# Optimization experiments

Hardware: AMD Instinct MI355X
Metric: run time of the kernel (lower is better)

Reference implementation:

```python
import jax, jax.numpy as jnp
import numpy as np

N_USER, N_SPOT, D = 100000, 50000, 128
E_VISIT, E_REV, E_NEAR = 500000, 500000, 200000
P_DROP = 0.1


def _glorot(k, fan_in, fan_out):
    lim = jnp.sqrt(6.0 / (fan_in + fan_out))
    return jax.random.uniform(k, (fan_in, fan_out), jnp.float32, -lim, lim)


def setup_inputs() -> dict:
    key = jax.random.key(0)
    ks = jax.random.split(key, 14)
    return {
        "x_user": jax.random.normal(ks[0], (N_USER, D), jnp.float32),
        "x_spot": jax.random.normal(ks[1], (N_SPOT, D), jnp.float32),
        "W_visit_src": _glorot(ks[2], D, D),   # user side of (user,visit,spot)
        "W_visit_tgt": _glorot(ks[3], D, D),   # spot side of (user,visit,spot)
        "W_rev_src": _glorot(ks[4], D, D),     # spot side of (spot,visited_by,user)
        "W_rev_tgt": _glorot(ks[5], D, D),     # user side of (spot,visited_by,user)
        "W_near_src": _glorot(ks[6], D, D),    # (spot,near,spot)
        "W_near_tgt": _glorot(ks[7], D, D),
        "visit_src": jax.random.randint(ks[8], (E_VISIT,), 0, N_USER, jnp.int64),
        "visit_dst": jax.random.randint(ks[9], (E_VISIT,), 0, N_SPOT, jnp.int64),
        "rev_src": jax.random.randint(ks[10], (E_REV,), 0, N_SPOT, jnp.int64),
        "rev_dst": jax.random.randint(ks[11], (E_REV,), 0, N_USER, jnp.int64),
        "near_src": jax.random.randint(ks[12], (E_NEAR,), 0, N_SPOT, jnp.int64),
        "near_dst": jax.random.randint(ks[13], (E_NEAR,), 0, N_SPOT, jnp.int64),
    }


def _scatter_mean(vals, idx, n_seg):
    # scatter(..., reduce='mean') into zeros: empty segments stay 0
    s = jax.ops.segment_sum(vals, idx, num_segments=n_seg)
    c = jax.ops.segment_sum(jnp.ones((vals.shape[0],), vals.dtype), idx, num_segments=n_seg)
    return s / jnp.maximum(c, 1.0)[:, None]


def _edge_type(x_src, x_tgt, W_src, W_tgt, src_idx, dst_idx, n_tgt, dkey):
    src_p = x_src @ W_src                      # [N_src, D]
    tgt_p = x_tgt @ W_tgt                      # [N_tgt, D]
    g = src_p[src_idx]                         # gather per edge [E, D]
    keep = jax.random.bernoulli(dkey, 1.0 - P_DROP, g.shape)
    g = jnp.where(keep, g / (1.0 - P_DROP), jnp.zeros_like(g))  # dropout (training)
    return tgt_p + _scatter_mean(g, dst_idx, n_tgt)


def reference(x_user, x_spot, W_visit_src, W_visit_tgt, W_rev_src, W_rev_tgt,
              W_near_src, W_near_tgt, visit_src, visit_dst, rev_src, rev_dst,
              near_src, near_dst):
    dk = jax.random.key(1)
    spot_a = _edge_type(x_user, x_spot, W_visit_src, W_visit_tgt,
                        visit_src, visit_dst, N_SPOT, jax.random.fold_in(dk, 0))
    user_a = _edge_type(x_spot, x_user, W_rev_src, W_rev_tgt,
                        rev_src, rev_dst, N_USER, jax.random.fold_in(dk, 1))
    spot_b = _edge_type(x_spot, x_spot, W_near_src, W_near_tgt,
                        near_src, near_dst, N_SPOT, jax.random.fold_in(dk, 2))
    # div: spot receives from 2 edge types, user from 1
    out_user = jax.nn.relu(user_a / 1.0)
    out_spot = jax.nn.relu((spot_a + spot_b) / 2.0)
    # ReLU=True applies a second relu (no-op after the first, kept for faithfulness)
    return jax.nn.relu(out_user), jax.nn.relu(out_spot)
```

## Files before the change

### kernel.cpp

```cpp
#include <hip/hip_runtime.h>
#include <stdint.h>

#define DF 128
typedef unsigned short ushort_t;
typedef __attribute__((ext_vector_type(8))) short short8v;
typedef __attribute__((ext_vector_type(4))) float f32x4;

__host__ __device__ __forceinline__ unsigned rotl32(unsigned v, int r) {
  return __builtin_rotateleft32(v, (unsigned)r);
}

__host__ __device__ __forceinline__ void threefry2x32(
    unsigned k0, unsigned k1, unsigned c0, unsigned c1,
    unsigned& o0, unsigned& o1) {
  unsigned kx = k0 ^ k1 ^ 0x1BD11BDAu;
  unsigned x0 = c0 + k0;
  unsigned x1 = c1 + k1;
#define TF_R(r) { x0 += x1; x1 = rotl32(x1, r); x1 ^= x0; }
  TF_R(13) TF_R(15) TF_R(26) TF_R(6)
  x0 += k1; x1 += kx + 1u;
  TF_R(17) TF_R(29) TF_R(16) TF_R(24)
  x0 += kx; x1 += k0 + 2u;
  TF_R(13) TF_R(15) TF_R(26) TF_R(6)
  x0 += k0; x1 += k1 + 3u;
  TF_R(17) TF_R(29) TF_R(16) TF_R(24)
  x0 += k1; x1 += kx + 4u;
  TF_R(13) TF_R(15) TF_R(26) TF_R(6)
  x0 += kx; x1 += k0 + 5u;
#undef TF_R
  o0 = x0; o1 = x1;
}

#define KEEP_THR 0xE6666600u

__device__ __forceinline__ ushort_t f2bf(float f) {
  unsigned u = __float_as_uint(f);
  unsigned r = (u + 0x7fffu + ((u >> 16) & 1u)) >> 16;
  return (ushort_t)r;
}
__device__ __forceinline__ float bf2f(unsigned h) {
  return __uint_as_float(h << 16);
}
__device__ __forceinline__ unsigned umin_u(unsigned a, unsigned b) {
  return a < b ? a : b;
}

#define WT(k, c) sm_u[(k) * 136 + (c)]
#define CTB(r, c) sm_u[(r) * 144 + (c)]
#define CTF(r, c) sm_f[(r) * 68 + (c)]

__device__ __forceinline__ void gemm_core(
    const float* __restrict__ X, const float* __restrict__ W1,
    const float* __restrict__ W2, bool sumW, int M, int rbase,
    ushort_t* sm_u, f32x4 acc[2][8]) {
  const int t = threadIdx.x;
  const int lane = t & 63;
  const int w = t >> 6;
  const int lr = lane & 15;
  const int kg = lane >> 4;

#pragma unroll
  for (int i = 0; i < 16; ++i) {
    int q = t + i * 256;
    int k = q >> 5;
    int c4 = (q & 31) * 4;
    float4 wv = *reinterpret_cast<const float4*>(&W1[k * DF + c4]);
    if (sumW) {
      float4 w2 = *reinterpret_cast<const float4*>(&W2[k * DF + c4]);
      wv.x += w2.x; wv.y += w2.y; wv.z += w2.z; wv.w += w2.w;
    }
    WT(c4 + 0, k) = f2bf(wv.x);
    WT(c4 + 1, k) = f2bf(wv.y);
    WT(c4 + 2, k) = f2bf(wv.z);
    WT(c4 + 3, k) = f2bf(wv.w);
  }
  __syncthreads();

#pragma unroll
  for (int rg = 0; rg < 2; ++rg)
#pragma unroll
    for (int n = 0; n < 8; ++n) acc[rg][n] = (f32x4){0.f, 0.f, 0.f, 0.f};

#pragma unroll
  for (int kt = 0; kt < 4; ++kt) {
    const int kb = kt * 32 + kg * 8;
    short8v a[2];
#pragma unroll
    for (int rg = 0; rg < 2; ++rg) {
      int r = rbase + w * 32 + rg * 16 + lr;
      float4 x0 = make_float4(0.f, 0.f, 0.f, 0.f);
      float4 x1 = x0;
      if (r < M) {
        x0 = *reinterpret_cast<const float4*>(&X[(size_t)r * DF + kb]);
        x1 = *reinterpret_cast<const float4*>(&X[(size_t)r * DF + kb + 4]);
      }
      short8v av;
      av[0] = (short)f2bf(x0.x); av[1] = (short)f2bf(x0.y);
      av[2] = (short)f2bf(x0.z); av[3] = (short)f2bf(x0.w);
      av[4] = (short)f2bf(x1.x); av[5] = (short)f2bf(x1.y);
      av[6] = (short)f2bf(x1.z); av[7] = (short)f2bf(x1.w);
      a[rg] = av;
    }
#pragma unroll
    for (int n = 0; n < 8; ++n) {
      short8v b = *reinterpret_cast<const short8v*>(&WT(n * 16 + lr, kb));
#pragma unroll
      for (int rg = 0; rg < 2; ++rg)
        acc[rg][n] = __builtin_amdgcn_mfma_f32_16x16x32_bf16(a[rg], b, acc[rg][n], 0, 0, 0);
    }
  }
}

__global__ __launch_bounds__(256) void proj3_gemm(
    const float* __restrict__ x_user, const float* __restrict__ x_spot,
    const float* __restrict__ Wv, const float* __restrict__ Wr,
    const float* __restrict__ Wn, int n_user, int n_spot,
    ushort_t* __restrict__ pv, ushort_t* __restrict__ pr,
    ushort_t* __restrict__ pn, int gbU, int gbS) {
  __shared__ __align__(16) ushort_t sm_u[18432];
  const int b = blockIdx.x;
  const float* X; const float* W; ushort_t* out; int M; int rbase;
  if (b < gbU)            { X = x_user; W = Wv; out = pv; M = n_user; rbase = b * 128; }
  else if (b < gbU + gbS) { X = x_spot; W = Wr; out = pr; M = n_spot; rbase = (b - gbU) * 128; }
  else                    { X = x_spot; W = Wn; out = pn; M = n_spot; rbase = (b - gbU - gbS) * 128; }

  f32x4 acc[2][8];
  gemm_core(X, W, nullptr, false, M, rbase, sm_u, acc);

  const int t = threadIdx.x;
  const int lane = t & 63;
  const int w = t >> 6;
  const int lr = lane & 15;
  const int kg = lane >> 4;

  __syncthreads();
#pragma unroll
  for (int rg = 0; rg < 2; ++rg) {
    const int rowb = w * 32 + rg * 16 + kg * 4;
#pragma unroll
    for (int n = 0; n < 8; ++n) {
      const int col = n * 16 + lr;
#pragma unroll
      for (int j = 0; j < 4; ++j) CTB(rowb + j, col) = f2bf(acc[rg][n][j]);
    }
  }
  __syncthreads();
#pragma unroll
  for (int i = 0; i < 8; ++i) {
    const int u = t + i * 256;
    const int row = u >> 4, ch = u & 15;
    const int grow = rbase + row;
    if (grow < M)
      *reinterpret_cast<uint4*>(&out[(size_t)grow * DF + ch * 8]) =
          *reinterpret_cast<const uint4*>(&CTB(row, ch * 8));
  }
}

__global__ __launch_bounds__(256) void final2_gemm(
    const float* __restrict__ x_user, const float* __restrict__ x_spot,
    const float* __restrict__ Wrt, const float* __restrict__ Wvt,
    const float* __restrict__ Wnt, int n_user, int n_spot,
    float* __restrict__ out_user, float* __restrict__ out_spot,
    const ushort_t* __restrict__ mean_u, const ushort_t* __restrict__ mean_sv,
    const ushort_t* __restrict__ mean_sn, int gbU) {
  __shared__ __align__(16) ushort_t sm_u[17408];
  float* sm_f_raw = reinterpret_cast<float*>(sm_u);
#define sm_f sm_f_raw
  const int b = blockIdx.x;
  const bool epi2 = (b >= gbU);
  const float* X; const float* W1; const float* W2; float* outF;
  const ushort_t* m1; const ushort_t* m2; int M; int rbase;
  if (!epi2) {
    X = x_user; W1 = Wrt; W2 = nullptr; outF = out_user;
    m1 = mean_u; m2 = nullptr; M = n_user; rbase = b * 128;
  } else {
    X = x_spot; W1 = Wvt; W2 = Wnt; outF = out_spot;
    m1 = mean_sv; m2 = mean_sn; M = n_spot; rbase = (b - gbU) * 128;
  }

  f32x4 acc[2][8];
  gemm_core(X, W1, W2, epi2, M, rbase, sm_u, acc);

  const int t = threadIdx.x;
  const int lane = t & 63;
  const int w = t >> 6;
  const int lr = lane & 15;
  const int kg = lane >> 4;

#pragma unroll
  for (int h = 0; h < 2; ++h) {
    __syncthreads();
#pragma unroll
    for (int rg = 0; rg < 2; ++rg) {
      const int rowb = w * 32 + rg * 16 + kg * 4;
#pragma unroll
      for (int n2 = 0; n2 < 4; ++n2) {
        const int n = h * 4 + n2;
        const int col = n2 * 16 + lr;
#pragma unroll
        for (int j = 0; j < 4; ++j) CTF(rowb + j, col) = acc[rg][n][j];
      }
    }
    __syncthreads();
#pragma unroll
    for (int i = 0; i < 8; ++i) {
      const int u = t + i * 256;
      const int row = u >> 4;
      const int c4 = (u & 15) * 4;
      const int grow = rbase + row;
      if (grow < M) {
        const float4 vv = *reinterpret_cast<const float4*>(&CTF(row, c4));
        const int col = h * 64 + c4;
        const uint2 mb = *reinterpret_cast<const uint2*>(&m1[(size_t)grow * DF + col]);
        float a0 = bf2f(mb.x & 0xffffu), a1 = bf2f(mb.x >> 16);
        float a2 = bf2f(mb.y & 0xffffu), a3 = bf2f(mb.y >> 16);
        float4 r;
        if (!epi2) {
          r.x = fmaxf(vv.x + a0, 0.f);
          r.y = fmaxf(vv.y + a1, 0.f);
          r.z = fmaxf(vv.z + a2, 0.f);
          r.w = fmaxf(vv.w + a3, 0.f);
        } else {
          const uint2 nb = *reinterpret_cast<const uint2*>(&m2[(size_t)grow * DF + col]);
          r.x = fmaxf(0.5f * (vv.x + a0 + bf2f(nb.x & 0xffffu)), 0.f);
          r.y = fmaxf(0.5f * (vv.y + a1 + bf2f(nb.x >> 16)), 0.f);
          r.z = fmaxf(0.5f * (vv.z + a2 + bf2f(nb.y & 0xffffu)), 0.f);
          r.w = fmaxf(0.5f * (vv.w + a3 + bf2f(nb.y >> 16)), 0.f);
        }
        *reinterpret_cast<float4*>(&outF[(size_t)grow * DF + col]) = r;
      }
    }
  }
#undef sm_f
}

__global__ __launch_bounds__(256) void hist3(
    const int* __restrict__ vd, const int* __restrict__ rd,
    const int* __restrict__ nd, unsigned* __restrict__ deg_all,
    int Ev, int Er, int En, int segU, int segN) {
  int i = blockIdx.x * 256 + threadIdx.x;
  if (i < Ev) atomicAdd(&deg_all[vd[i]], 1u);
  else if (i < Ev + Er) atomicAdd(&deg_all[segU + rd[i - Ev]], 1u);
  else if (i < Ev + Er + En) atomicAdd(&deg_all[segN + nd[i - Ev - Er]], 1u);
}

#define SCAN_E 2048

__global__ __launch_bounds__(256) void scanA(
    const unsigned* __restrict__ deg, unsigned* __restrict__ bsum, int NT) {
  __shared__ unsigned sm[256];
  const int t = threadIdx.x;
  const int base = blockIdx.x * SCAN_E + t * 8;
  unsigned s = 0;
#pragma unroll
  for (int j = 0; j < 8; ++j) {
    int i = base + j;
    s += (i < NT) ? deg[i] : 0u;
  }
  sm[t] = s;
  __syncthreads();
  for (int off = 128; off; off >>= 1) {
    if (t < off) sm[t] += sm[t + off];
    __syncthreads();
  }
  if (t == 0) bsum[blockIdx.x] = sm[0];
}

__global__ __launch_bounds__(1024) void scanB(
    unsigned* __restrict__ bsum, unsigned* __restrict__ rp_all,
    int nb, int NT) {
  __shared__ unsigned sm[1024];
  const int t = threadIdx.x;
  unsigned v = (t < nb) ? bsum[t] : 0u;
  sm[t] = v;
  __syncthreads();
  for (int off = 1; off < 1024; off <<= 1) {
    unsigned u = (t >= off) ? sm[t - off] : 0u;
    __syncthreads();
    sm[t] += u;
    __syncthreads();
  }
  if (t < nb) bsum[t] = sm[t] - v;
  if (t == nb - 1) rp_all[NT] = sm[t];
}

__global__ __launch_bounds__(256) void scanC(
    const unsigned* __restrict__ deg, const unsigned* __restrict__ bsum,
    unsigned* __restrict__ rp, unsigned* __restrict__ cur, int NT) {
  __shared__ unsigned sm[256];
  const int t = threadIdx.x;
  const int base = blockIdx.x * SCAN_E + t * 8;
  unsigned vals[8];
  unsigned s = 0;
#pragma unroll
  for (int j = 0; j < 8; ++j) {
    int i = base + j;
    vals[j] = (i < NT) ? deg[i] : 0u;
    s += vals[j];
  }
  sm[t] = s;
  __syncthreads();
  for (int off = 1; off < 256; off <<= 1) {
    unsigned u = (t >= off) ? sm[t - off] : 0u;
    __syncthreads();
    sm[t] += u;
    __syncthreads();
  }
  unsigned run = bsum[blockIdx.x] + sm[t] - s;
#pragma unroll
  for (int j = 0; j < 8; ++j) {
    int i = base + j;
    if (i < NT) { rp[i] = run; cur[i] = run; }
    run += vals[j];
  }
}

__global__ __launch_bounds__(256) void fill3(
    const int* __restrict__ vs, const int* __restrict__ vd,
    const int* __restrict__ rs, const int* __restrict__ rd,
    const int* __restrict__ ns, const int* __restrict__ nd,
    unsigned* __restrict__ cur_all, uint2* __restrict__ es_all,
    int Ev, int Er, int En, int segU, int segN) {
  int i = blockIdx.x * 256 + threadIdx.x;
  if (i < Ev) {
    unsigned slot = atomicAdd(&cur_all[vd[i]], 1u);
    es_all[slot] = make_uint2((unsigned)i, (unsigned)vs[i]);
  } else if (i < Ev + Er) {
    int e = i - Ev;
    unsigned slot = atomicAdd(&cur_all[segU + rd[e]], 1u);
    es_all[slot] = make_uint2((unsigned)e, (unsigned)rs[e]);
  } else if (i < Ev + Er + En) {
    int e = i - Ev - Er;
    unsigned slot = atomicAdd(&cur_all[segN + nd[e]], 1u);
    es_all[slot] = make_uint2((unsigned)e, (unsigned)ns[e]);
  }
}

__global__ __launch_bounds__(256) void gather_reduce_all(
    const ushort_t* __restrict__ proj_v, const ushort_t* __restrict__ proj_r,
    const ushort_t* __restrict__ proj_n, const uint2* __restrict__ es,
    const unsigned* __restrict__ rp, ushort_t* __restrict__ accum_all,
    int NT, int segU, int segN, unsigned emax,
    unsigned kv0, unsigned kv1, unsigned kr0, unsigned kr1,
    unsigned kn0, unsigned kn1) {
  const int lane = threadIdx.x & 63;
  int d = blockIdx.x * 4 + (threadIdx.x >> 6);
  d = __builtin_amdgcn_readfirstlane(d);
  if (d >= NT) return;

  const ushort_t* proj;
  unsigned k0, k1;
  if (d < segU)      { proj = proj_v; k0 = kv0; k1 = kv1; }
  else if (d < segN) { proj = proj_r; k0 = kr0; k1 = kr1; }
  else               { proj = proj_n; k0 = kn0; k1 = kn1; }

  const unsigned b0 = __builtin_amdgcn_readfirstlane(rp[d]);
  const unsigned n  = __builtin_amdgcn_readfirstlane(rp[d + 1]) - b0;

  const bool hi = lane >= 32;
  const unsigned l31 = (unsigned)(lane & 31);
  const unsigned voff8 = l31 * 8u;

  const unsigned npairs = n >> 1;
  const unsigned odd = n & 1u;

  uint2 P0 = es[umin_u(b0, emax)];
  uint2 P1 = es[umin_u(b0 + 1u, emax)];
  unsigned eA = __builtin_amdgcn_readfirstlane(P0.x);
  unsigned sA = __builtin_amdgcn_readfirstlane(P0.y);
  unsigned eB = __builtin_amdgcn_readfirstlane(P1.x);
  unsigned sB = __builtin_amdgcn_readfirstlane(P1.y);

  float a0 = 0.f, a1 = 0.f, a2 = 0.f, a3 = 0.f;

  for (unsigned p = 0; p < npairs; ++p) {
    const unsigned src = hi ? sB : sA;
    const unsigned eid = hi ? eB : eA;
    const uint2 g = *reinterpret_cast<const uint2*>(
        reinterpret_cast<const char*>(proj) + ((size_t)src << 8) + voff8);
    uint2 Pn0 = es[umin_u(b0 + 2u * p + 2u, emax)];
    uint2 Pn1 = es[umin_u(b0 + 2u * p + 3u, emax)];

    const unsigned cb = eid * 128u + l31 * 4u;
    unsigned r0a, r0b, r1a, r1b, r2a, r2b, r3a, r3b;
    threefry2x32(k0, k1, 0u, cb + 0u, r0a, r0b);
    threefry2x32(k0, k1, 0u, cb + 1u, r1a, r1b);
    threefry2x32(k0, k1, 0u, cb + 2u, r2a, r2b);
    threefry2x32(k0, k1, 0u, cb + 3u, r3a, r3b);
    const float m0 = ((r0a ^ r0b) < KEEP_THR) ? (1.0f / 0.9f) : 0.f;
    const float m1 = ((r1a ^ r1b) < KEEP_THR) ? (1.0f / 0.9f) : 0.f;
    const float m2 = ((r2a ^ r2b) < KEEP_THR) ? (1.0f / 0.9f) : 0.f;
    const float m3 = ((r3a ^ r3b) < KEEP_THR) ? (1.0f / 0.9f) : 0.f;
    a0 = fmaf(__uint_as_float(g.x << 16), m0, a0);
    a1 = fmaf(__uint_as_float(g.x & 0xffff0000u), m1, a1);
    a2 = fmaf(__uint_as_float(g.y << 16), m2, a2);
    a3 = fmaf(__uint_as_float(g.y & 0xffff0000u), m3, a3);

    eA = __builtin_amdgcn_readfirstlane(Pn0.x);
    sA = __builtin_amdgcn_readfirstlane(Pn0.y);
    eB = __builtin_amdgcn_readfirstlane(Pn1.x);
    sB = __builtin_amdgcn_readfirstlane(Pn1.y);
  }

  if (odd) {
    const uint2 g = *reinterpret_cast<const uint2*>(
        reinterpret_cast<const char*>(proj) + ((size_t)sA << 8) + voff8);
    const unsigned cb = eA * 128u + l31 * 4u;
    unsigned r0a, r0b, r1a, r1b, r2a, r2b, r3a, r3b;
    threefry2x32(k0, k1, 0u, cb + 0u, r0a, r0b);
    threefry2x32(k0, k1, 0u, cb + 1u, r1a, r1b);
    threefry2x32(k0, k1, 0u, cb + 2u, r2a, r2b);
    threefry2x32(k0, k1, 0u, cb + 3u, r3a, r3b);
    const float sc = hi ? 0.f : (1.0f / 0.9f);
    const float m0 = ((r0a ^ r0b) < KEEP_THR) ? sc : 0.f;
    const float m1 = ((r1a ^ r1b) < KEEP_THR) ? sc : 0.f;
    const float m2 = ((r2a ^ r2b) < KEEP_THR) ? sc : 0.f;
    const float m3 = ((r3a ^ r3b) < KEEP_THR) ? sc : 0.f;
    a0 = fmaf(__uint_as_float(g.x << 16), m0, a0);
    a1 = fmaf(__uint_as_float(g.x & 0xffff0000u), m1, a1);
    a2 = fmaf(__uint_as_float(g.y << 16), m2, a2);
    a3 = fmaf(__uint_as_float(g.y & 0xffff0000u), m3, a3);
  }

  a0 += __shfl_xor(a0, 32);
  a1 += __shfl_xor(a1, 32);
  a2 += __shfl_xor(a2, 32);
  a3 += __shfl_xor(a3, 32);

  const float inv = 1.0f / fmaxf((float)n, 1.0f);
  const float u0 = hi ? a2 : a0;
  const float u1 = hi ? a3 : a1;
  const unsigned pk =
      ((unsigned)f2bf(u0 * inv)) | (((unsigned)f2bf(u1 * inv)) << 16);
  unsigned* out = reinterpret_cast<unsigned*>(accum_all) + (size_t)d * 64;
  out[2u * l31 + (hi ? 1u : 0u)] = pk;
}

extern "C" void kernel_launch(void* const* d_in, const int* in_sizes, int n_in,
                              void* d_out, int out_size, void* d_ws, size_t ws_size,
                              hipStream_t stream) {
  const float* x_user      = (const float*)d_in[0];
  const float* x_spot      = (const float*)d_in[1];
  const float* W_visit_src = (const float*)d_in[2];
  const float* W_visit_tgt = (const float*)d_in[3];
  const float* W_rev_src   = (const float*)d_in[4];
  const float* W_rev_tgt   = (const float*)d_in[5];
  const float* W_near_src  = (const float*)d_in[6];
  const float* W_near_tgt  = (const float*)d_in[7];
  const int* visit_src = (const int*)d_in[8];
  const int* visit_dst = (const int*)d_in[9];
  const int* rev_src   = (const int*)d_in[10];
  const int* rev_dst   = (const int*)d_in[11];
  const int* near_src  = (const int*)d_in[12];
  const int* near_dst  = (const int*)d_in[13];

  const int n_user = in_sizes[0] / DF;
  const int n_spot = in_sizes[1] / DF;
  const int e_visit = in_sizes[8];
  const int e_rev   = in_sizes[10];
  const int e_near  = in_sizes[12];

  float* out_user = (float*)d_out;
  float* out_spot = out_user + (size_t)n_user * DF;

  const int NT = n_spot + n_user + n_spot;
  const int segU = n_spot;
  const int segN = n_spot + n_user;
  const int etot = e_visit + e_rev + e_near;
  const unsigned emax = (unsigned)(etot - 1);

  char* ws = (char*)d_ws;
  size_t off = 0;
  auto alloc = [&](size_t bytes) -> void* {
    void* p = ws + off;
    off += (bytes + 255) & ~(size_t)255;
    return p;
  };
  ushort_t* proj_vs   = (ushort_t*)alloc((size_t)n_user * DF * 2);
  ushort_t* proj_rs   = (ushort_t*)alloc((size_t)n_spot * DF * 2);
  ushort_t* proj_ns   = (ushort_t*)alloc((size_t)n_spot * DF * 2);
  ushort_t* accum_all = (ushort_t*)alloc((size_t)NT * DF * 2);
  uint2*    es_all    = (uint2*)   alloc((size_t)etot * 8);
  unsigned* rp_all    = (unsigned*)alloc(((size_t)NT + 1) * 4);
  unsigned* cur_all   = (unsigned*)alloc((size_t)NT * 4);
  unsigned* deg_all   = (unsigned*)alloc((size_t)NT * 4);
  unsigned* bsum      = (unsigned*)alloc(4096);

  ushort_t* mean_sv = accum_all;
  ushort_t* mean_u  = accum_all + (size_t)segU * DF;
  ushort_t* mean_sn = accum_all + (size_t)segN * DF;

  unsigned kv0, kv1, kr0, kr1, kn0, kn1;
  threefry2x32(0u, 1u, 0u, 0u, kv0, kv1);
  threefry2x32(0u, 1u, 0u, 1u, kr0, kr1);
  threefry2x32(0u, 1u, 0u, 2u, kn0, kn1);

  dim3 blk(256);
  const int gbU = (n_user + 127) / 128;
  const int gbS = (n_spot + 127) / 128;
  const int gb_e = (etot + 255) / 256;
  const int nb_scan = (NT + SCAN_E - 1) / SCAN_E;

  hipMemsetAsync(deg_all, 0, (size_t)NT * 4, stream);
  hist3<<<gb_e, blk, 0, stream>>>(visit_dst, rev_dst, near_dst, deg_all,
                                  e_visit, e_rev, e_near, segU, segN);
  scanA<<<nb_scan, blk, 0, stream>>>(deg_all, bsum, NT);
  scanB<<<1, 1024, 0, stream>>>(bsum, rp_all, nb_scan, NT);
  scanC<<<nb_scan, blk, 0, stream>>>(deg_all, bsum, rp_all, cur_all, NT);
  fill3<<<gb_e, blk, 0, stream>>>(visit_src, visit_dst, rev_src, rev_dst,
                                  near_src, near_dst, cur_all, es_all,
                                  e_visit, e_rev, e_near, segU, segN);

  proj3_gemm<<<gbU + 2 * gbS, blk, 0, stream>>>(
      x_user, x_spot, W_visit_src, W_rev_src, W_near_src,
      n_user, n_spot, proj_vs, proj_rs, proj_ns, gbU, gbS);

  gather_reduce_all<<<(NT + 3) / 4, blk, 0, stream>>>(
      proj_vs, proj_rs, proj_ns, es_all, rp_all, accum_all,
      NT, segU, segN, emax, kv0, kv1, kr0, kr1, kn0, kn1);

  final2_gemm<<<gbU + gbS, blk, 0, stream>>>(
      x_user, x_spot, W_rev_tgt, W_visit_tgt, W_near_tgt,
      n_user, n_spot, out_user, out_spot, mean_u, mean_sv, mean_sn, gbU);
}
```

Baseline: 559.9 us.

## Fuse histogram into projection GEMM, merge scan passes, simplify gather loop

```diff
diff --git a/kernel.cpp b/kernel.cpp
--- a/kernel.cpp
+++ b/kernel.cpp
@@ -41,9 +41,6 @@
 __device__ __forceinline__ float bf2f(unsigned h) {
   return __uint_as_float(h << 16);
 }
-__device__ __forceinline__ unsigned umin_u(unsigned a, unsigned b) {
-  return a < b ? a : b;
-}
 
 #define WT(k, c) sm_u[(k) * 136 + (c)]
 #define CTB(r, c) sm_u[(r) * 144 + (c)]
@@ -111,14 +108,26 @@
   }
 }
 
-__global__ __launch_bounds__(256) void proj3_gemm(
+__global__ __launch_bounds__(256) void proj3_hist(
     const float* __restrict__ x_user, const float* __restrict__ x_spot,
     const float* __restrict__ Wv, const float* __restrict__ Wr,
     const float* __restrict__ Wn, int n_user, int n_spot,
     ushort_t* __restrict__ pv, ushort_t* __restrict__ pr,
-    ushort_t* __restrict__ pn, int gbU, int gbS) {
+    ushort_t* __restrict__ pn, int gbU, int gbS,
+    const int* __restrict__ vd, const int* __restrict__ rd,
+    const int* __restrict__ nd, unsigned* __restrict__ deg_all,
+    int Ev, int Er, int En, int segU, int segN, int gemmBlocks) {
   __shared__ __align__(16) ushort_t sm_u[18432];
   const int b = blockIdx.x;
+
+  if (b >= gemmBlocks) {
+    int i = (b - gemmBlocks) * 256 + threadIdx.x;
+    if (i < Ev) atomicAdd(&deg_all[vd[i]], 1u);
+    else if (i < Ev + Er) atomicAdd(&deg_all[segU + rd[i - Ev]], 1u);
+    else if (i < Ev + Er + En) atomicAdd(&deg_all[segN + nd[i - Ev - Er]], 1u);
+    return;
+  }
+
   const float* X; const float* W; ushort_t* out; int M; int rbase;
   if (b < gbU)            { X = x_user; W = Wv; out = pv; M = n_user; rbase = b * 128; }
   else if (b < gbU + gbS) { X = x_spot; W = Wr; out = pr; M = n_spot; rbase = (b - gbU) * 128; }
@@ -234,21 +243,14 @@
 #undef sm_f
 }
 
-__global__ __launch_bounds__(256) void hist3(
-    const int* __restrict__ vd, const int* __restrict__ rd,
-    const int* __restrict__ nd, unsigned* __restrict__ deg_all,
-    int Ev, int Er, int En, int segU, int segN) {
-  int i = blockIdx.x * 256 + threadIdx.x;
-  if (i < Ev) atomicAdd(&deg_all[vd[i]], 1u);
-  else if (i < Ev + Er) atomicAdd(&deg_all[segU + rd[i - Ev]], 1u);
-  else if (i < Ev + Er + En) atomicAdd(&deg_all[segN + nd[i - Ev - Er]], 1u);
-}
-
 #define SCAN_E 2048
 
-__global__ __launch_bounds__(256) void scanA(
-    const unsigned* __restrict__ deg, unsigned* __restrict__ bsum, int NT) {
+__global__ __launch_bounds__(256) void scanAB(
+    const unsigned* __restrict__ deg, unsigned* __restrict__ bsum,
+    unsigned* __restrict__ rp_all, unsigned* __restrict__ done,
+    int NT, int nb) {
   __shared__ unsigned sm[256];
+  __shared__ int amLast;
   const int t = threadIdx.x;
   const int base = blockIdx.x * SCAN_E + t * 8;
   unsigned s = 0;
@@ -263,25 +265,28 @@
     if (t < off) sm[t] += sm[t + off];
     __syncthreads();
   }
-  if (t == 0) bsum[blockIdx.x] = sm[0];
-}
-
-__global__ __launch_bounds__(1024) void scanB(
-    unsigned* __restrict__ bsum, unsigned* __restrict__ rp_all,
-    int nb, int NT) {
-  __shared__ unsigned sm[1024];
-  const int t = threadIdx.x;
-  unsigned v = (t < nb) ? bsum[t] : 0u;
-  sm[t] = v;
+  if (t == 0) {
+    bsum[blockIdx.x] = sm[0];
+    __threadfence();
+    unsigned prev = atomicAdd(done, 1u);
+    amLast = (prev == (unsigned)(nb - 1));
+  }
   __syncthreads();
-  for (int off = 1; off < 1024; off <<= 1) {
-    unsigned u = (t >= off) ? sm[t - off] : 0u;
-    __syncthreads();
-    sm[t] += u;
-    __syncthreads();
-  }
-  if (t < nb) bsum[t] = sm[t] - v;
-  if (t == nb - 1) rp_all[NT] = sm[t];
+  if (amLast) {
+    __threadfence();
+    unsigned v = (t < nb) ? bsum[t] : 0u;
+    __syncthreads();
+    sm[t] = v;
+    __syncthreads();
+    for (int off = 1; off < 256; off <<= 1) {
+      unsigned u = (t >= off) ? sm[t - off] : 0u;
+      __syncthreads();
+      sm[t] += u;
+      __syncthreads();
+    }
+    if (t < nb) bsum[t] = sm[t] - v;
+    if (t == nb - 1) rp_all[NT] = sm[t];
+  }
 }
 
 __global__ __launch_bounds__(256) void scanC(
@@ -357,61 +362,34 @@
   const unsigned b0 = __builtin_amdgcn_readfirstlane(rp[d]);
   const unsigned n  = __builtin_amdgcn_readfirstlane(rp[d + 1]) - b0;
 
-  const bool hi = lane >= 32;
+  const unsigned hiadd = (unsigned)lane >> 5;
   const unsigned l31 = (unsigned)(lane & 31);
   const unsigned voff8 = l31 * 8u;
-
-  const unsigned npairs = n >> 1;
-  const unsigned odd = n & 1u;
-
-  uint2 P0 = es[umin_u(b0, emax)];
-  uint2 P1 = es[umin_u(b0 + 1u, emax)];
-  unsigned eA = __builtin_amdgcn_readfirstlane(P0.x);
-  unsigned sA = __builtin_amdgcn_readfirstlane(P0.y);
-  unsigned eB = __builtin_amdgcn_readfirstlane(P1.x);
-  unsigned sB = __builtin_amdgcn_readfirstlane(P1.y);
+  const unsigned niter = (n + 1u) >> 1;
+
+  const char* es_c = reinterpret_cast<const char*>(es);
+  const char* proj_c = reinterpret_cast<const char*>(proj);
+
+  unsigned idx = min(b0 + hiadd, emax);
+  uint2 E = *reinterpret_cast<const uint2*>(es_c + (size_t)(idx * 8u));
 
   float a0 = 0.f, a1 = 0.f, a2 = 0.f, a3 = 0.f;
 
-  for (unsigned p = 0; p < npairs; ++p) {
-    const unsigned src = hi ? sB : sA;
-    const unsigned eid = hi ? eB : eA;
+  for (unsigned p = 0; p < niter; ++p) {
+    const unsigned eid = E.x;
+    const unsigned src = E.y;
+    unsigned nidx = min(b0 + 2u * p + 2u + hiadd, emax);
+    uint2 En = *reinterpret_cast<const uint2*>(es_c + (size_t)(nidx * 8u));
     const uint2 g = *reinterpret_cast<const uint2*>(
-        reinterpret_cast<const char*>(proj) + ((size_t)src << 8) + voff8);
-    uint2 Pn0 = es[umin_u(b0 + 2u * p + 2u, emax)];
-    uint2 Pn1 = es[umin_u(b0 + 2u * p + 3u, emax)];
-
-    const unsigned cb = eid * 128u + l31 * 4u;
+        proj_c + (size_t)((src << 8) + voff8));
+    const float sc = (2u * p + hiadd < n) ? (1.0f / 0.9f) : 0.f;
+
+    const unsigned cb = (eid << 7) + l31 * 4u;
     unsigned r0a, r0b, r1a, r1b, r2a, r2b, r3a, r3b;
     threefry2x32(k0, k1, 0u, cb + 0u, r0a, r0b);
     threefry2x32(k0, k1, 0u, cb + 1u, r1a, r1b);
     threefry2x32(k0, k1, 0u, cb + 2u, r2a, r2b);
     threefry2x32(k0, k1, 0u, cb + 3u, r3a, r3b);
-    const float m0 = ((r0a ^ r0b) < KEEP_THR) ? (1.0f / 0.9f) : 0.f;
-    const float m1 = ((r1a ^ r1b) < KEEP_THR) ? (1.0f / 0.9f) : 0.f;
-    const float m2 = ((r2a ^ r2b) < KEEP_THR) ? (1.0f / 0.9f) : 0.f;
-    const float m3 = ((r3a ^ r3b) < KEEP_THR) ? (1.0f / 0.9f) : 0.f;
-    a0 = fmaf(__uint_as_float(g.x << 16), m0, a0);
-    a1 = fmaf(__uint_as_float(g.x & 0xffff0000u), m1, a1);
-    a2 = fmaf(__uint_as_float(g.y << 16), m2, a2);
-    a3 = fmaf(__uint_as_float(g.y & 0xffff0000u), m3, a3);
-
-    eA = __builtin_amdgcn_readfirstlane(Pn0.x);
-    sA = __builtin_amdgcn_readfirstlane(Pn0.y);
-    eB = __builtin_amdgcn_readfirstlane(Pn1.x);
-    sB = __builtin_amdgcn_readfirstlane(Pn1.y);
-  }
-
-  if (odd) {
-    const uint2 g = *reinterpret_cast<const uint2*>(
-        reinterpret_cast<const char*>(proj) + ((size_t)sA << 8) + voff8);
-    const unsigned cb = eA * 128u + l31 * 4u;
-    unsigned r0a, r0b, r1a, r1b, r2a, r2b, r3a, r3b;
-    threefry2x32(k0, k1, 0u, cb + 0u, r0a, r0b);
-    threefry2x32(k0, k1, 0u, cb + 1u, r1a, r1b);
-    threefry2x32(k0, k1, 0u, cb + 2u, r2a, r2b);
-    threefry2x32(k0, k1, 0u, cb + 3u, r3a, r3b);
-    const float sc = hi ? 0.f : (1.0f / 0.9f);
     const float m0 = ((r0a ^ r0b) < KEEP_THR) ? sc : 0.f;
     const float m1 = ((r1a ^ r1b) < KEEP_THR) ? sc : 0.f;
     const float m2 = ((r2a ^ r2b) < KEEP_THR) ? sc : 0.f;
@@ -420,6 +398,8 @@
     a1 = fmaf(__uint_as_float(g.x & 0xffff0000u), m1, a1);
     a2 = fmaf(__uint_as_float(g.y << 16), m2, a2);
     a3 = fmaf(__uint_as_float(g.y & 0xffff0000u), m3, a3);
+
+    E = En;
   }
 
   a0 += __shfl_xor(a0, 32);
@@ -428,12 +408,12 @@
   a3 += __shfl_xor(a3, 32);
 
   const float inv = 1.0f / fmaxf((float)n, 1.0f);
-  const float u0 = hi ? a2 : a0;
-  const float u1 = hi ? a3 : a1;
+  const float u0 = hiadd ? a2 : a0;
+  const float u1 = hiadd ? a3 : a1;
   const unsigned pk =
       ((unsigned)f2bf(u0 * inv)) | (((unsigned)f2bf(u1 * inv)) << 16);
   unsigned* out = reinterpret_cast<unsigned*>(accum_all) + (size_t)d * 64;
-  out[2u * l31 + (hi ? 1u : 0u)] = pk;
+  out[2u * l31 + hiadd] = pk;
 }
 
 extern "C" void kernel_launch(void* const* d_in, const int* in_sizes, int n_in,
@@ -484,7 +464,9 @@
   unsigned* rp_all    = (unsigned*)alloc(((size_t)NT + 1) * 4);
   unsigned* cur_all   = (unsigned*)alloc((size_t)NT * 4);
   unsigned* deg_all   = (unsigned*)alloc((size_t)NT * 4);
+  unsigned* done      = (unsigned*)alloc(256);
   unsigned* bsum      = (unsigned*)alloc(4096);
+  char* zero_end = (char*)bsum;
 
   ushort_t* mean_sv = accum_all;
   ushort_t* mean_u  = accum_all + (size_t)segU * DF;
@@ -500,21 +482,22 @@
   const int gbS = (n_spot + 127) / 128;
   const int gb_e = (etot + 255) / 256;
   const int nb_scan = (NT + SCAN_E - 1) / SCAN_E;
-
-  hipMemsetAsync(deg_all, 0, (size_t)NT * 4, stream);
-  hist3<<<gb_e, blk, 0, stream>>>(visit_dst, rev_dst, near_dst, deg_all,
-                                  e_visit, e_rev, e_near, segU, segN);
-  scanA<<<nb_scan, blk, 0, stream>>>(deg_all, bsum, NT);
-  scanB<<<1, 1024, 0, stream>>>(bsum, rp_all, nb_scan, NT);
+  const int gemmBlocks = gbU + 2 * gbS;
+
+  hipMemsetAsync(deg_all, 0, (size_t)(zero_end - (char*)deg_all), stream);
+
+  proj3_hist<<<gemmBlocks + gb_e, blk, 0, stream>>>(
+      x_user, x_spot, W_visit_src, W_rev_src, W_near_src,
+      n_user, n_spot, proj_vs, proj_rs, proj_ns, gbU, gbS,
+      visit_dst, rev_dst, near_dst, deg_all,
+      e_visit, e_rev, e_near, segU, segN, gemmBlocks);
+
+  scanAB<<<nb_scan, blk, 0, stream>>>(deg_all, bsum, rp_all, done, NT, nb_scan);
   scanC<<<nb_scan, blk, 0, stream>>>(deg_all, bsum, rp_all, cur_all, NT);
   fill3<<<gb_e, blk, 0, stream>>>(visit_src, visit_dst, rev_src, rev_dst,
                                   near_src, near_dst, cur_all, es_all,
                                   e_visit, e_rev, e_near, segU, segN);
 
-  proj3_gemm<<<gbU + 2 * gbS, blk, 0, stream>>>(
-      x_user, x_spot, W_visit_src, W_rev_src, W_near_src,
-      n_user, n_spot, proj_vs, proj_rs, proj_ns, gbU, gbS);
-
   gather_reduce_all<<<(NT + 3) / 4, blk, 0, stream>>>(
       proj_vs, proj_rs, proj_ns, es_all, rp_all, accum_all,
       NT, segU, segN, emax, kv0, kv1, kr0, kr1, kn0, kn1);
```

After: 557.3 us. No clear change (-0.5%).

## Fuse degree histogram into projection GEMM and merge scan passes into one kernel

Applied to the files above, without the earlier changes.

```diff
diff --git a/kernel.cpp b/kernel.cpp
--- a/kernel.cpp
+++ b/kernel.cpp
@@ -111,14 +111,26 @@
   }
 }
 
-__global__ __launch_bounds__(256) void proj3_gemm(
+__global__ __launch_bounds__(256) void proj3_hist(
     const float* __restrict__ x_user, const float* __restrict__ x_spot,
     const float* __restrict__ Wv, const float* __restrict__ Wr,
     const float* __restrict__ Wn, int n_user, int n_spot,
     ushort_t* __restrict__ pv, ushort_t* __restrict__ pr,
-    ushort_t* __restrict__ pn, int gbU, int gbS) {
+    ushort_t* __restrict__ pn, int gbU, int gbS,
+    const int* __restrict__ vd, const int* __restrict__ rd,
+    const int* __restrict__ nd, unsigned* __restrict__ deg_all,
+    int Ev, int Er, int En, int segU, int segN, int gemmBlocks) {
   __shared__ __align__(16) ushort_t sm_u[18432];
   const int b = blockIdx.x;
+
+  if (b >= gemmBlocks) {
+    int i = (b - gemmBlocks) * 256 + threadIdx.x;
+    if (i < Ev) atomicAdd(&deg_all[vd[i]], 1u);
+    else if (i < Ev + Er) atomicAdd(&deg_all[segU + rd[i - Ev]], 1u);
+    else if (i < Ev + Er + En) atomicAdd(&deg_all[segN + nd[i - Ev - Er]], 1u);
+    return;
+  }
+
   const float* X; const float* W; ushort_t* out; int M; int rbase;
   if (b < gbU)            { X = x_user; W = Wv; out = pv; M = n_user; rbase = b * 128; }
   else if (b < gbU + gbS) { X = x_spot; W = Wr; out = pr; M = n_spot; rbase = (b - gbU) * 128; }
@@ -234,60 +246,15 @@
 #undef sm_f
 }
 
-__global__ __launch_bounds__(256) void hist3(
-    const int* __restrict__ vd, const int* __restrict__ rd,
-    const int* __restrict__ nd, unsigned* __restrict__ deg_all,
-    int Ev, int Er, int En, int segU, int segN) {
-  int i = blockIdx.x * 256 + threadIdx.x;
-  if (i < Ev) atomicAdd(&deg_all[vd[i]], 1u);
-  else if (i < Ev + Er) atomicAdd(&deg_all[segU + rd[i - Ev]], 1u);
-  else if (i < Ev + Er + En) atomicAdd(&deg_all[segN + nd[i - Ev - Er]], 1u);
-}
-
 #define SCAN_E 2048
 
-__global__ __launch_bounds__(256) void scanA(
-    const unsigned* __restrict__ deg, unsigned* __restrict__ bsum, int NT) {
+__global__ __launch_bounds__(256) void scanABC(
+    const unsigned* __restrict__ deg, unsigned* __restrict__ bsum,
+    unsigned* __restrict__ bsumX, unsigned* __restrict__ rp,
+    unsigned* __restrict__ cur, unsigned* __restrict__ done,
+    int NT, int nb) {
   __shared__ unsigned sm[256];
-  const int t = threadIdx.x;
-  const int base = blockIdx.x * SCAN_E + t * 8;
-  unsigned s = 0;
-#pragma unroll
-  for (int j = 0; j < 8; ++j) {
-    int i = base + j;
-    s += (i < NT) ? deg[i] : 0u;
-  }
-  sm[t] = s;
-  __syncthreads();
-  for (int off = 128; off; off >>= 1) {
-    if (t < off) sm[t] += sm[t + off];
-    __syncthreads();
-  }
-  if (t == 0) bsum[blockIdx.x] = sm[0];
-}
-
-__global__ __launch_bounds__(1024) void scanB(
-    unsigned* __restrict__ bsum, unsigned* __restrict__ rp_all,
-    int nb, int NT) {
-  __shared__ unsigned sm[1024];
-  const int t = threadIdx.x;
-  unsigned v = (t < nb) ? bsum[t] : 0u;
-  sm[t] = v;
-  __syncthreads();
-  for (int off = 1; off < 1024; off <<= 1) {
-    unsigned u = (t >= off) ? sm[t - off] : 0u;
-    __syncthreads();
-    sm[t] += u;
-    __syncthreads();
-  }
-  if (t < nb) bsum[t] = sm[t] - v;
-  if (t == nb - 1) rp_all[NT] = sm[t];
-}
-
-__global__ __launch_bounds__(256) void scanC(
-    const unsigned* __restrict__ deg, const unsigned* __restrict__ bsum,
-    unsigned* __restrict__ rp, unsigned* __restrict__ cur, int NT) {
-  __shared__ unsigned sm[256];
+  __shared__ int amLast;
   const int t = threadIdx.x;
   const int base = blockIdx.x * SCAN_E + t * 8;
   unsigned vals[8];
@@ -306,7 +273,47 @@
     sm[t] += u;
     __syncthreads();
   }
-  unsigned run = bsum[blockIdx.x] + sm[t] - s;
+  const unsigned myExcl = sm[t] - s;
+  const unsigned blockTotal = sm[255];
+
+  if (t == 0) {
+    bsum[blockIdx.x] = blockTotal;
+    __threadfence();
+    unsigned prev = atomicAdd(&done[0], 1u);
+    amLast = (prev == (unsigned)(nb - 1));
+  }
+  __syncthreads();
+
+  if (amLast) {
+    __threadfence();
+    unsigned v = (t < nb) ? bsum[t] : 0u;
+    __syncthreads();
+    sm[t] = v;
+    __syncthreads();
+    for (int off = 1; off < 256; off <<= 1) {
+      unsigned u = (t >= off) ? sm[t - off] : 0u;
+      __syncthreads();
+      sm[t] += u;
+      __syncthreads();
+    }
+    if (t < nb) bsumX[t] = sm[t] - v;
+    if (t == nb - 1) rp[NT] = sm[t];
+    __threadfence();
+    if (t == 0) __hip_atomic_store(&done[1], 1u, __ATOMIC_RELEASE,
+                                   __HIP_MEMORY_SCOPE_AGENT);
+  }
+
+  if (t == 0) {
+    while (__hip_atomic_load(&done[1], __ATOMIC_ACQUIRE,
+                             __HIP_MEMORY_SCOPE_AGENT) == 0u) {
+      __builtin_amdgcn_s_sleep(8);
+    }
+  }
+  __syncthreads();
+
+  const unsigned bx = __hip_atomic_load(&bsumX[blockIdx.x], __ATOMIC_RELAXED,
+                                        __HIP_MEMORY_SCOPE_AGENT);
+  unsigned run = bx + myExcl;
 #pragma unroll
   for (int j = 0; j < 8; ++j) {
     int i = base + j;
@@ -484,7 +491,10 @@
   unsigned* rp_all    = (unsigned*)alloc(((size_t)NT + 1) * 4);
   unsigned* cur_all   = (unsigned*)alloc((size_t)NT * 4);
   unsigned* deg_all   = (unsigned*)alloc((size_t)NT * 4);
+  unsigned* done      = (unsigned*)alloc(256);
   unsigned* bsum      = (unsigned*)alloc(4096);
+  unsigned* bsumX     = (unsigned*)alloc(4096);
+  char* zero_end = (char*)bsum;
 
   ushort_t* mean_sv = accum_all;
   ushort_t* mean_u  = accum_all + (size_t)segU * DF;
@@ -500,21 +510,22 @@
   const int gbS = (n_spot + 127) / 128;
   const int gb_e = (etot + 255) / 256;
   const int nb_scan = (NT + SCAN_E - 1) / SCAN_E;
-
-  hipMemsetAsync(deg_all, 0, (size_t)NT * 4, stream);
-  hist3<<<gb_e, blk, 0, stream>>>(visit_dst, rev_dst, near_dst, deg_all,
-                                  e_visit, e_rev, e_near, segU, segN);
-  scanA<<<nb_scan, blk, 0, stream>>>(deg_all, bsum, NT);
-  scanB<<<1, 1024, 0, stream>>>(bsum, rp_all, nb_scan, NT);
-  scanC<<<nb_scan, blk, 0, stream>>>(deg_all, bsum, rp_all, cur_all, NT);
+  const int gemmBlocks = gbU + 2 * gbS;
+
+  hipMemsetAsync(deg_all, 0, (size_t)(zero_end - (char*)deg_all), stream);
+
+  proj3_hist<<<gemmBlocks + gb_e, blk, 0, stream>>>(
+      x_user, x_spot, W_visit_src, W_rev_src, W_near_src,
+      n_user, n_spot, proj_vs, proj_rs, proj_ns, gbU, gbS,
+      visit_dst, rev_dst, near_dst, deg_all,
+      e_visit, e_rev, e_near, segU, segN, gemmBlocks);
+
+  scanABC<<<nb_scan, blk, 0, stream>>>(deg_all, bsum, bsumX, rp_all, cur_all,
+                                       done, NT, nb_scan);
   fill3<<<gb_e, blk, 0, stream>>>(visit_src, visit_dst, rev_src, rev_dst,
                                   near_src, near_dst, cur_all, es_all,
                                   e_visit, e_rev, e_near, segU, segN);
 
-  proj3_gemm<<<gbU + 2 * gbS, blk, 0, stream>>>(
-      x_user, x_spot, W_visit_src, W_rev_src, W_near_src,
-      n_user, n_spot, proj_vs, proj_rs, proj_ns, gbU, gbS);
-
   gather_reduce_all<<<(NT + 3) / 4, blk, 0, stream>>>(
       proj_vs, proj_rs, proj_ns, es_all, rp_all, accum_all,
       NT, segU, segN, emax, kv0, kv1, kr0, kr1, kn0, kn1);
```

New measurement: 530.5 us, median of 2. -5.3%, faster.
